# Kernel tuning notes

Hardware: AMD Instinct MI355X
Metric: run time of the kernel (lower is better)

The kernel has to match this reference:

```python
import jax, jax.numpy as jnp
import numpy as np

N, L, D = 256, 512, 512


def _attention(x, W_in, W_out, apply_tanh):
    # x: [N, L, D]; 'general' attention: project query, score against context (=x)
    q = jnp.einsum('bld,ed->ble', x, W_in)          # [N, L, D]
    scores = jnp.einsum('bld,bmd->blm', q, x)       # [N, L, L]
    w = jax.nn.softmax(scores, axis=-1)             # softmax over keys
    mix = jnp.einsum('blm,bmd->bld', w, x)          # [N, L, D]
    comb = jnp.concatenate([mix, q], axis=-1)       # [N, L, 2D]
    out = jnp.einsum('blc,dc->bld', comb, W_out)    # Linear(2D, D), no bias
    return jnp.tanh(out) if apply_tanh else out


def setup_inputs() -> dict:
    key = jax.random.key(0)
    k1, k2, k3, k4, k5 = jax.random.split(key, 5)
    s = 0.02
    return {
        'embeddings': jax.random.normal(k1, (N, L, D), dtype=jnp.float32),
        'W_in1': jax.random.normal(k2, (D, D), dtype=jnp.float32) * s,
        'W_out1': jax.random.normal(k3, (D, 2 * D), dtype=jnp.float32) * s,
        'W_in2': jax.random.normal(k4, (D, D), dtype=jnp.float32) * s,
        'W_out2': jax.random.normal(k5, (D, 2 * D), dtype=jnp.float32) * s,
    }


def reference(embeddings, W_in1, W_out1, W_in2, W_out2):
    x = _attention(embeddings, W_in1, W_out1, apply_tanh=True)   # block 1 (tanh)
    x = _attention(x, W_in2, W_out2, apply_tanh=False)           # block 2 (no tanh)
    # transpose(1,2) + avg_pool1d over full length == mean over L
    pooled = jnp.mean(x, axis=1)                                  # [N, D]
    return pooled.reshape(pooled.shape[0], -1, 1, 1)              # [N, D, 1, 1]
```

## Files before the change

### kernel.cpp

```cpp
#include <hip/hip_runtime.h>
#include <cstdint>
#include <cstddef>

typedef uint16_t u16;
typedef __attribute__((ext_vector_type(8))) short bf16x8;
typedef __attribute__((ext_vector_type(4))) float f32x4;
typedef __attribute__((ext_vector_type(4))) uint16_t u16x4;

#define GLOBAL_AS(p) (const __attribute__((address_space(1))) void*)(p)
#define LDS_AS(p)    (__attribute__((address_space(3))) void*)(p)

__device__ __forceinline__ u16 f2b(float f){
  uint32_t u = __float_as_uint(f);
  u += 0x7fff + ((u >> 16) & 1);
  return (u16)(u >> 16);
}
__device__ __forceinline__ float b2f(u16 h){
  return __uint_as_float(((uint32_t)h) << 16);
}

__global__ void cvt_bf16_kernel(const float* __restrict__ src, u16* __restrict__ dst, int n){
  int i = (blockIdx.x * 256 + threadIdx.x) * 4;
  if (i >= n) return;
  float4 f = *(const float4*)(src + i);
  u16x4 o; o.x = f2b(f.x); o.y = f2b(f.y); o.z = f2b(f.z); o.w = f2b(f.w);
  *(u16x4*)(dst + i) = o;
}

__global__ void cvtT_kernel(const float* __restrict__ src, u16* __restrict__ x, u16* __restrict__ xT){
  __shared__ u16 tile[64][68];
  size_t b = blockIdx.y;
  int t = blockIdx.x;
  int r0 = (t >> 3) * 64, c0 = (t & 7) * 64;
  const float* s = src + b * 262144;
  u16* dx = x + b * 262144;
  u16* dT = xT + b * 262144;
  int tx = threadIdx.x & 63, ty = threadIdx.x >> 6;
  #pragma unroll
  for (int k = 0; k < 16; k++){
    int r = ty * 16 + k;
    u16 v = f2b(s[(size_t)(r0 + r) * 512 + c0 + tx]);
    dx[(size_t)(r0 + r) * 512 + c0 + tx] = v;
    tile[r][tx] = v;
  }
  __syncthreads();
  #pragma unroll
  for (int k = 0; k < 16; k++){
    int c = ty * 16 + k;
    dT[(size_t)(c0 + c) * 512 + r0 + tx] = tile[tx][c];
  }
}

__global__ void transpose512_kernel(const u16* __restrict__ src, u16* __restrict__ dst){
  __shared__ u16 tile[64][68];
  size_t b = blockIdx.y;
  int t = blockIdx.x;
  int r0 = (t >> 3) * 64, c0 = (t & 7) * 64;
  const u16* s = src + b * 262144;
  u16* d = dst + b * 262144;
  int tx = threadIdx.x & 63, ty = threadIdx.x >> 6;
  #pragma unroll
  for (int k = 0; k < 16; k++){
    int r = ty * 16 + k;
    tile[r][tx] = s[(size_t)(r0 + r) * 512 + c0 + tx];
  }
  __syncthreads();
  #pragma unroll
  for (int k = 0; k < 16; k++){
    int c = ty * 16 + k;
    d[(size_t)(c0 + c) * 512 + r0 + tx] = tile[tx][c];
  }
}

__global__ void softmax_kernel(const float* __restrict__ S, u16* __restrict__ P){
  int row = blockIdx.x * 4 + (threadIdx.x >> 6);
  int lane = threadIdx.x & 63;
  const float* s = S + (size_t)row * 512;
  float v[8];
  float mx = -3.0e38f;
  #pragma unroll
  for (int i = 0; i < 8; i++){ v[i] = s[lane + i * 64]; mx = fmaxf(mx, v[i]); }
  #pragma unroll
  for (int o = 32; o > 0; o >>= 1) mx = fmaxf(mx, __shfl_xor(mx, o));
  float sum = 0.f;
  #pragma unroll
  for (int i = 0; i < 8; i++){ v[i] = __expf(v[i] - mx); sum += v[i]; }
  #pragma unroll
  for (int o = 32; o > 0; o >>= 1) sum += __shfl_xor(sum, o);
  float inv = 1.0f / sum;
  u16* p = P + (size_t)row * 512;
  #pragma unroll
  for (int i = 0; i < 8; i++) p[lane + i * 64] = f2b(v[i] * inv);
}

template<bool SPLIT, bool TANH, bool POOL, typename CT>
__global__ __launch_bounds__(256, 2) void gemm_bt_kernel(
    const u16* __restrict__ A0, const u16* __restrict__ A1,
    const u16* __restrict__ B, CT* __restrict__ C,
    int K, int ldb, int64_t aBatch, int64_t bBatch, int64_t cBatch,
    float* __restrict__ poolOut, int b0)
{
  __shared__ __align__(16) u16 As[128 * 32];
  __shared__ __align__(16) u16 Bs[128 * 32];
  int64_t bat = blockIdx.y;
  int m0 = (blockIdx.x >> 2) * 128, n0 = (blockIdx.x & 3) * 128;
  A0 += bat * aBatch;
  if (SPLIT) A1 += bat * aBatch;
  B += bat * bBatch;
  if (!POOL) C += bat * cBatch;
  int tid = threadIdx.x, lane = tid & 63;
  int w = tid >> 6;
  int wm = (w >> 1) * 64, wn = (w & 1) * 64;
  f32x4 acc[4][4];
  #pragma unroll
  for (int i = 0; i < 4; i++)
    #pragma unroll
    for (int j = 0; j < 4; j++) acc[i][j] = (f32x4){0.f, 0.f, 0.f, 0.f};

  int sRow = tid >> 2, sCol = (tid & 3) * 8;
  int fr = lane & 15, fq = (lane >> 4) * 8;

  for (int k0 = 0; k0 < K; k0 += 32){
    const u16* Ap = A0; int kk = k0;
    if (SPLIT && k0 >= 512){ Ap = A1; kk = k0 - 512; }
    const u16* ga = Ap + (size_t)(m0 + sRow) * 512 + kk + sCol;
    const u16* gb = B  + (size_t)(n0 + sRow) * ldb + k0 + sCol;
    __builtin_amdgcn_global_load_lds(GLOBAL_AS(ga),                    LDS_AS(&As[tid * 8]),        16, 0, 0);
    __builtin_amdgcn_global_load_lds(GLOBAL_AS(ga + (size_t)64 * 512), LDS_AS(&As[2048 + tid * 8]), 16, 0, 0);
    __builtin_amdgcn_global_load_lds(GLOBAL_AS(gb),                    LDS_AS(&Bs[tid * 8]),        16, 0, 0);
    __builtin_amdgcn_global_load_lds(GLOBAL_AS(gb + (size_t)64 * ldb), LDS_AS(&Bs[2048 + tid * 8]), 16, 0, 0);
    __syncthreads();
    bf16x8 af[4], bfr[4];
    #pragma unroll
    for (int i = 0; i < 4; i++) af[i]  = *(const bf16x8*)&As[(wm + i * 16 + fr) * 32 + fq];
    #pragma unroll
    for (int j = 0; j < 4; j++) bfr[j] = *(const bf16x8*)&Bs[(wn + j * 16 + fr) * 32 + fq];
    #pragma unroll
    for (int i = 0; i < 4; i++)
      #pragma unroll
      for (int j = 0; j < 4; j++)
        acc[i][j] = __builtin_amdgcn_mfma_f32_16x16x32_bf16(af[i], bfr[j], acc[i][j], 0, 0, 0);
    __syncthreads();
  }

  if constexpr (POOL){
    #pragma unroll
    for (int j = 0; j < 4; j++){
      float p = 0.f;
      #pragma unroll
      for (int i = 0; i < 4; i++)
        #pragma unroll
        for (int r = 0; r < 4; r++) p += acc[i][j][r];
      p += __shfl_xor(p, 16);
      p += __shfl_xor(p, 32);
      if (lane < 16){
        int col = n0 + wn + j * 16 + lane;
        atomicAdd(poolOut + ((size_t)(b0) + bat) * 512 + col, p * (1.0f / 512.0f));
      }
    }
  } else {
    int cq = (lane >> 4) * 4, cc = lane & 15;
    #pragma unroll
    for (int i = 0; i < 4; i++){
      #pragma unroll
      for (int j = 0; j < 4; j++){
        #pragma unroll
        for (int r = 0; r < 4; r++){
          int row = m0 + wm + i * 16 + cq + r;
          int col = n0 + wn + j * 16 + cc;
          float v = acc[i][j][r];
          if (TANH) v = tanhf(v);
          if constexpr (sizeof(CT) == 4) C[(size_t)row * 512 + col] = v;
          else                           C[(size_t)row * 512 + col] = f2b(v);
        }
      }
    }
  }
}

extern "C" void kernel_launch(void* const* d_in, const int* in_sizes, int n_in,
                              void* d_out, int out_size, void* d_ws, size_t ws_size,
                              hipStream_t stream) {
  const float* emb   = (const float*)d_in[0];
  const float* Win1  = (const float*)d_in[1];
  const float* Wout1 = (const float*)d_in[2];
  const float* Win2  = (const float*)d_in[3];
  const float* Wout2 = (const float*)d_in[4];
  float* out = (float*)d_out;

  int CB = 256;
  while (CB > 1 && (4ull << 20) + (size_t)CB * (3ull << 20) > ws_size) CB >>= 1;
  const int64_t E = 262144;

  char* wsb = (char*)d_ws;
  u16* Win1b  = (u16*)wsb;
  u16* Wout1b = Win1b + 262144;
  u16* Win2b  = Wout1b + 524288;
  u16* Wout2b = Win2b + 262144;
  u16* base = (u16*)(wsb + (4 << 20));
  u16*   Ar  = base;
  u16*   Br  = base + (size_t)CB * E;
  u16*   Cr  = base + 2 * (size_t)CB * E;
  float* Dr  = (float*)(base + 3 * (size_t)CB * E);
  u16*   Fr  = base + 5 * (size_t)CB * E;

  hipMemsetAsync(d_out, 0, (size_t)out_size * sizeof(float), stream);

  cvt_bf16_kernel<<<256, 256, 0, stream>>>(Win1,  Win1b,  262144);
  cvt_bf16_kernel<<<512, 256, 0, stream>>>(Wout1, Wout1b, 524288);
  cvt_bf16_kernel<<<256, 256, 0, stream>>>(Win2,  Win2b,  262144);
  cvt_bf16_kernel<<<512, 256, 0, stream>>>(Wout2, Wout2b, 524288);

  dim3 gg(16, CB);
  dim3 gt(64, CB);

  for (int c = 0; c < 256 / CB; c++){
    const float* embc = emb + (size_t)c * CB * 262144;
    int b0 = c * CB;

    cvtT_kernel<<<gt, 256, 0, stream>>>(embc, Ar, Cr);
    gemm_bt_kernel<false,false,false,u16><<<gg, 256, 0, stream>>>(
        Ar, nullptr, Win1b, Br, 512, 512, E, 0, E, nullptr, 0);
    gemm_bt_kernel<false,false,false,float><<<gg, 256, 0, stream>>>(
        Br, nullptr, Ar, Dr, 512, 512, E, E, 262144, nullptr, 0);
    softmax_kernel<<<CB * 128, 256, 0, stream>>>(Dr, Fr);
    gemm_bt_kernel<false,false,false,u16><<<gg, 256, 0, stream>>>(
        Fr, nullptr, Cr, Ar, 512, 512, E, E, E, nullptr, 0);
    gemm_bt_kernel<true,true,false,u16><<<gg, 256, 0, stream>>>(
        Ar, Br, Wout1b, Cr, 1024, 1024, E, 0, E, nullptr, 0);

    gemm_bt_kernel<false,false,false,u16><<<gg, 256, 0, stream>>>(
        Cr, nullptr, Win2b, Br, 512, 512, E, 0, E, nullptr, 0);
    transpose512_kernel<<<gt, 256, 0, stream>>>(Cr, Fr);
    gemm_bt_kernel<false,false,false,float><<<gg, 256, 0, stream>>>(
        Br, nullptr, Cr, Dr, 512, 512, E, E, 262144, nullptr, 0);
    softmax_kernel<<<CB * 128, 256, 0, stream>>>(Dr, Ar);
    gemm_bt_kernel<false,false,false,u16><<<gg, 256, 0, stream>>>(
        Ar, nullptr, Fr, Cr, 512, 512, E, E, E, nullptr, 0);
    gemm_bt_kernel<true,false,true,u16><<<gg, 256, 0, stream>>>(
        Cr, Br, Wout2b, (u16*)nullptr, 1024, 1024, E, 0, 0, out, b0);
  }
}
```

Measured before the change: 1.887 ms.

## Fuse QK^T, softmax and PV into a single attention kernel per block

Replaces the separate score GEMM, fp32 score store, softmax kernel and PV GEMM with one attn_kernel. Each workgroup keeps 64 query rows resident in LDS, computes full 512-wide scores in registers, does a cross-wave softmax through a small LDS stats buffer, writes the probabilities back into LDS as bf16, and then multiplies them by the transposed context. This removes the round trip of the fp32 score matrix and the bf16 probability matrix through global memory. It also swaps the GEMM block-index mapping, reorders the buffer use, and shrinks the workspace requirement. In exchange it uses large LDS and register footprints at occupancy 1 with only 8 blocks per batch.

```diff
diff --git a/kernel.cpp b/kernel.cpp
--- a/kernel.cpp
+++ b/kernel.cpp
@@ -72,25 +72,151 @@
   }
 }
 
-__global__ void softmax_kernel(const float* __restrict__ S, u16* __restrict__ P){
-  int row = blockIdx.x * 4 + (threadIdx.x >> 6);
-  int lane = threadIdx.x & 63;
-  const float* s = S + (size_t)row * 512;
-  float v[8];
-  float mx = -3.0e38f;
-  #pragma unroll
-  for (int i = 0; i < 8; i++){ v[i] = s[lane + i * 64]; mx = fmaxf(mx, v[i]); }
-  #pragma unroll
-  for (int o = 32; o > 0; o >>= 1) mx = fmaxf(mx, __shfl_xor(mx, o));
-  float sum = 0.f;
-  #pragma unroll
-  for (int i = 0; i < 8; i++){ v[i] = __expf(v[i] - mx); sum += v[i]; }
-  #pragma unroll
-  for (int o = 32; o > 0; o >>= 1) sum += __shfl_xor(sum, o);
-  float inv = 1.0f / sum;
-  u16* p = P + (size_t)row * 512;
-  #pragma unroll
-  for (int i = 0; i < 8; i++) p[lane + i * 64] = f2b(v[i] * inv);
+__global__ __launch_bounds__(256, 1) void attn_kernel(
+    const u16* __restrict__ q, const u16* __restrict__ x, const u16* __restrict__ xT,
+    u16* __restrict__ mix)
+{
+  __shared__ __align__(16) u16 U[64 * 520];
+  __shared__ __align__(16) u16 Bx[512 * 32];
+  __shared__ float stats[2][64][4];
+  const int64_t E = 262144;
+  int64_t bat = blockIdx.y;
+  q += bat * E; x += bat * E; xT += bat * E; mix += bat * E;
+  int m0 = blockIdx.x * 64;
+  int tid = threadIdx.x, lane = tid & 63, w = tid >> 6;
+  int fr = lane & 15, qd = lane >> 4, fq = qd * 8;
+
+  #pragma unroll
+  for (int c = 0; c < 16; c++){
+    int id = c * 256 + tid;
+    int row = id >> 6, cb = id & 63;
+    *(bf16x8*)&U[row * 520 + cb * 8] =
+        *(const bf16x8*)(q + (size_t)(m0 + row) * 512 + cb * 8);
+  }
+
+  f32x4 acc[4][8];
+  #pragma unroll
+  for (int i = 0; i < 4; i++)
+    #pragma unroll
+    for (int j = 0; j < 8; j++) acc[i][j] = (f32x4){0.f, 0.f, 0.f, 0.f};
+
+  for (int k0 = 0; k0 < 512; k0 += 32){
+    #pragma unroll
+    for (int s = 0; s < 8; s++){
+      const u16* g = x + (size_t)(s * 64 + (tid >> 2)) * 512 + k0 + (tid & 3) * 8;
+      __builtin_amdgcn_global_load_lds(GLOBAL_AS(g), LDS_AS(&Bx[s * 2048 + tid * 8]), 16, 0, 0);
+    }
+    __syncthreads();
+    bf16x8 af[4], bfr[8];
+    #pragma unroll
+    for (int i = 0; i < 4; i++) af[i]  = *(const bf16x8*)&U[(i * 16 + fr) * 520 + k0 + fq];
+    #pragma unroll
+    for (int j = 0; j < 8; j++) bfr[j] = *(const bf16x8*)&Bx[(w * 128 + j * 16 + fr) * 32 + fq];
+    #pragma unroll
+    for (int i = 0; i < 4; i++)
+      #pragma unroll
+      for (int j = 0; j < 8; j++)
+        acc[i][j] = __builtin_amdgcn_mfma_f32_16x16x32_bf16(af[i], bfr[j], acc[i][j], 0, 0, 0);
+    __syncthreads();
+  }
+
+  float mfull[4][4], inv[4][4];
+  #pragma unroll
+  for (int i = 0; i < 4; i++)
+    #pragma unroll
+    for (int r = 0; r < 4; r++){
+      float m = acc[i][0][r];
+      #pragma unroll
+      for (int j = 1; j < 8; j++) m = fmaxf(m, acc[i][j][r]);
+      #pragma unroll
+      for (int o = 1; o <= 8; o <<= 1) m = fmaxf(m, __shfl_xor(m, o));
+      mfull[i][r] = m;
+    }
+  if (fr == 0){
+    #pragma unroll
+    for (int i = 0; i < 4; i++)
+      #pragma unroll
+      for (int r = 0; r < 4; r++) stats[0][i * 16 + qd * 4 + r][w] = mfull[i][r];
+  }
+  __syncthreads();
+  #pragma unroll
+  for (int i = 0; i < 4; i++)
+    #pragma unroll
+    for (int r = 0; r < 4; r++){
+      int row = i * 16 + qd * 4 + r;
+      float m = fmaxf(fmaxf(stats[0][row][0], stats[0][row][1]),
+                      fmaxf(stats[0][row][2], stats[0][row][3]));
+      mfull[i][r] = m;
+      float s = 0.f;
+      #pragma unroll
+      for (int j = 0; j < 8; j++){
+        float e = __expf(acc[i][j][r] - m);
+        acc[i][j][r] = e; s += e;
+      }
+      #pragma unroll
+      for (int o = 1; o <= 8; o <<= 1) s += __shfl_xor(s, o);
+      inv[i][r] = s;
+    }
+  if (fr == 0){
+    #pragma unroll
+    for (int i = 0; i < 4; i++)
+      #pragma unroll
+      for (int r = 0; r < 4; r++) stats[1][i * 16 + qd * 4 + r][w] = inv[i][r];
+  }
+  __syncthreads();
+  #pragma unroll
+  for (int i = 0; i < 4; i++)
+    #pragma unroll
+    for (int r = 0; r < 4; r++){
+      int row = i * 16 + qd * 4 + r;
+      inv[i][r] = 1.0f / (stats[1][row][0] + stats[1][row][1] +
+                          stats[1][row][2] + stats[1][row][3]);
+    }
+  #pragma unroll
+  for (int i = 0; i < 4; i++)
+    #pragma unroll
+    for (int r = 0; r < 4; r++)
+      #pragma unroll
+      for (int j = 0; j < 8; j++){
+        int row = i * 16 + qd * 4 + r;
+        int col = w * 128 + j * 16 + fr;
+        uint32_t mine = f2b(acc[i][j][r] * inv[i][r]);
+        uint32_t oth = (uint32_t)__shfl_xor((int)mine, 1);
+        if (!(fr & 1)) *(uint32_t*)&U[row * 520 + col] = mine | (oth << 16);
+      }
+  __syncthreads();
+
+  #pragma unroll
+  for (int i = 0; i < 4; i++)
+    #pragma unroll
+    for (int j = 0; j < 8; j++) acc[i][j] = (f32x4){0.f, 0.f, 0.f, 0.f};
+  for (int k0 = 0; k0 < 512; k0 += 32){
+    #pragma unroll
+    for (int s = 0; s < 8; s++){
+      const u16* g = xT + (size_t)(s * 64 + (tid >> 2)) * 512 + k0 + (tid & 3) * 8;
+      __builtin_amdgcn_global_load_lds(GLOBAL_AS(g), LDS_AS(&Bx[s * 2048 + tid * 8]), 16, 0, 0);
+    }
+    __syncthreads();
+    bf16x8 af[4], bfr[8];
+    #pragma unroll
+    for (int i = 0; i < 4; i++) af[i]  = *(const bf16x8*)&U[(i * 16 + fr) * 520 + k0 + fq];
+    #pragma unroll
+    for (int j = 0; j < 8; j++) bfr[j] = *(const bf16x8*)&Bx[(w * 128 + j * 16 + fr) * 32 + fq];
+    #pragma unroll
+    for (int i = 0; i < 4; i++)
+      #pragma unroll
+      for (int j = 0; j < 8; j++)
+        acc[i][j] = __builtin_amdgcn_mfma_f32_16x16x32_bf16(af[i], bfr[j], acc[i][j], 0, 0, 0);
+    __syncthreads();
+  }
+  #pragma unroll
+  for (int i = 0; i < 4; i++)
+    #pragma unroll
+    for (int j = 0; j < 8; j++)
+      #pragma unroll
+      for (int r = 0; r < 4; r++)
+        mix[(size_t)(m0 + i * 16 + qd * 4 + r) * 512 + w * 128 + j * 16 + fr] =
+            f2b(acc[i][j][r]);
 }
 
 template<bool SPLIT, bool TANH, bool POOL, typename CT>
@@ -103,7 +229,7 @@
   __shared__ __align__(16) u16 As[128 * 32];
   __shared__ __align__(16) u16 Bs[128 * 32];
   int64_t bat = blockIdx.y;
-  int m0 = (blockIdx.x >> 2) * 128, n0 = (blockIdx.x & 3) * 128;
+  int m0 = (blockIdx.x & 3) * 128, n0 = (blockIdx.x >> 2) * 128;
   A0 += bat * aBatch;
   if (SPLIT) A1 += bat * aBatch;
   B += bat * bBatch;
@@ -189,7 +315,7 @@
   float* out = (float*)d_out;
 
   int CB = 256;
-  while (CB > 1 && (4ull << 20) + (size_t)CB * (3ull << 20) > ws_size) CB >>= 1;
+  while (CB > 1 && (4ull << 20) + (size_t)CB * (5ull * 524288ull) > ws_size) CB >>= 1;
   const int64_t E = 262144;
 
   char* wsb = (char*)d_ws;
@@ -198,11 +324,11 @@
   u16* Win2b  = Wout1b + 524288;
   u16* Wout2b = Win2b + 262144;
   u16* base = (u16*)(wsb + (4 << 20));
-  u16*   Ar  = base;
-  u16*   Br  = base + (size_t)CB * E;
-  u16*   Cr  = base + 2 * (size_t)CB * E;
-  float* Dr  = (float*)(base + 3 * (size_t)CB * E);
-  u16*   Fr  = base + 5 * (size_t)CB * E;
+  u16* Ar = base;
+  u16* Br = base + (size_t)CB * E;
+  u16* Cr = base + 2 * (size_t)CB * E;
+  u16* Dr = base + 3 * (size_t)CB * E;
+  u16* Fr = base + 4 * (size_t)CB * E;
 
   hipMemsetAsync(d_out, 0, (size_t)out_size * sizeof(float), stream);
 
@@ -212,6 +338,7 @@
   cvt_bf16_kernel<<<512, 256, 0, stream>>>(Wout2, Wout2b, 524288);
 
   dim3 gg(16, CB);
+  dim3 ga(8, CB);
   dim3 gt(64, CB);
 
   for (int c = 0; c < 256 / CB; c++){
@@ -221,23 +348,15 @@
     cvtT_kernel<<<gt, 256, 0, stream>>>(embc, Ar, Cr);
     gemm_bt_kernel<false,false,false,u16><<<gg, 256, 0, stream>>>(
         Ar, nullptr, Win1b, Br, 512, 512, E, 0, E, nullptr, 0);
-    gemm_bt_kernel<false,false,false,float><<<gg, 256, 0, stream>>>(
-        Br, nullptr, Ar, Dr, 512, 512, E, E, 262144, nullptr, 0);
-    softmax_kernel<<<CB * 128, 256, 0, stream>>>(Dr, Fr);
+    attn_kernel<<<ga, 256, 0, stream>>>(Br, Ar, Cr, Fr);
+    gemm_bt_kernel<true,true,false,u16><<<gg, 256, 0, stream>>>(
+        Fr, Br, Wout1b, Dr, 1024, 1024, E, 0, E, nullptr, 0);
+
+    transpose512_kernel<<<gt, 256, 0, stream>>>(Dr, Cr);
     gemm_bt_kernel<false,false,false,u16><<<gg, 256, 0, stream>>>(
-        Fr, nullptr, Cr, Ar, 512, 512, E, E, E, nullptr, 0);
-    gemm_bt_kernel<true,true,false,u16><<<gg, 256, 0, stream>>>(
-        Ar, Br, Wout1b, Cr, 1024, 1024, E, 0, E, nullptr, 0);
-
-    gemm_bt_kernel<false,false,false,u16><<<gg, 256, 0, stream>>>(
-        Cr, nullptr, Win2b, Br, 512, 512, E, 0, E, nullptr, 0);
-    transpose512_kernel<<<gt, 256, 0, stream>>>(Cr, Fr);
-    gemm_bt_kernel<false,false,false,float><<<gg, 256, 0, stream>>>(
-        Br, nullptr, Cr, Dr, 512, 512, E, E, 262144, nullptr, 0);
-    softmax_kernel<<<CB * 128, 256, 0, stream>>>(Dr, Ar);
-    gemm_bt_kernel<false,false,false,u16><<<gg, 256, 0, stream>>>(
-        Ar, nullptr, Fr, Cr, 512, 512, E, E, E, nullptr, 0);
+        Dr, nullptr, Win2b, Ar, 512, 512, E, 0, E, nullptr, 0);
+    attn_kernel<<<ga, 256, 0, stream>>>(Ar, Dr, Cr, Fr);
     gemm_bt_kernel<true,false,true,u16><<<gg, 256, 0, stream>>>(
-        Cr, Br, Wout2b, (u16*)nullptr, 1024, 1024, E, 0, 0, out, b0);
-  }
-}
+        Fr, Ar, Wout2b, (u16*)nullptr, 1024, 1024, E, 0, 0, out, b0);
+  }
+}
```

Result: slower. 1.967 ms (+4.3%).
